# Kernel optimization log

Measured on AMD Instinct MI355X. Metric: run time of the kernel, lower is better.

The kernel has to match this reference:

```python
import jax, jax.numpy as jnp
import numpy as np

B = 16          # number of point clouds
N_COARSE = 1024  # points per cloud at coarse level
N_FINE = 4096    # points per cloud at fine level
C_IN = 256       # coarse feature channels
C_SKIP = 128     # fine skip feature channels
C_HID = 256
EPS = 1e-16


def setup_inputs() -> dict:
    key = jax.random.key(0)
    ks = jax.random.split(key, 8)
    x = jax.random.normal(ks[0], (B * N_COARSE, C_IN), dtype=jnp.float32)
    pos = jax.random.uniform(ks[1], (B * N_COARSE, 3), dtype=jnp.float32)
    x_skip = jax.random.normal(ks[2], (B * N_FINE, C_SKIP), dtype=jnp.float32)
    pos_skip = jax.random.uniform(ks[3], (B * N_FINE, 3), dtype=jnp.float32)
    # uniform batch assignment (sorted), one segment per cloud
    batch = jnp.repeat(jnp.arange(B, dtype=jnp.int32), N_COARSE)
    batch_skip = jnp.repeat(jnp.arange(B, dtype=jnp.int32), N_FINE)
    # MLP params: Linear(384 -> 256) + ReLU, Linear(256 -> 256) + ReLU
    c0 = C_IN + C_SKIP
    W1 = jax.random.normal(ks[4], (c0, C_HID), dtype=jnp.float32) / np.sqrt(c0)
    b1 = jnp.zeros((C_HID,), dtype=jnp.float32)
    W2 = jax.random.normal(ks[5], (C_HID, C_HID), dtype=jnp.float32) / np.sqrt(C_HID)
    b2 = jnp.zeros((C_HID,), dtype=jnp.float32)
    return {"x": x, "pos": pos, "x_skip": x_skip, "pos_skip": pos_skip,
            "W1": W1, "b1": b1, "W2": W2, "b2": b2,
            "batch": batch, "batch_skip": batch_skip, "k": 3}


def _knn_interpolate(x, pos, pos_skip, k):
    # batch is uniform: reshape into [B, n, ...] blocks (same as per-batch kNN)
    xb = x.reshape(B, N_COARSE, -1)          # [B, Nc, C]
    pc = pos.reshape(B, N_COARSE, 3)         # [B, Nc, 3]
    pf = pos_skip.reshape(B, N_FINE, 3)      # [B, Nf, 3]
    # squared pairwise distances within each cloud: [B, Nf, Nc]
    d2 = jnp.sum((pf[:, :, None, :] - pc[:, None, :, :]) ** 2, axis=-1)
    neg_d2, idx = jax.lax.top_k(-d2, k)      # k nearest -> [B, Nf, k]
    w = 1.0 / jnp.maximum(-neg_d2, EPS)      # inverse-squared-distance weights
    gathered = jax.vmap(lambda xc, i: xc[i])(xb, idx)  # [B, Nf, k, C]
    interp = jnp.sum(w[..., None] * gathered, axis=2) / jnp.sum(w, axis=2, keepdims=True)
    return interp.reshape(B * N_FINE, -1)    # [B*Nf, C]


def reference(x, pos, x_skip, pos_skip, W1, b1, W2, b2, batch, batch_skip, k):
    x_up = _knn_interpolate(x, pos, pos_skip, k)
    h = jnp.concatenate([x_up, x_skip], axis=1)          # [B*Nf, C_IN+C_SKIP]
    h = jax.nn.relu(h @ W1 + b1)
    h = jax.nn.relu(h @ W2 + b2)
    return (h, pos_skip, batch_skip)
```

## Files before the change

### kernel.cpp

```cpp
#include <hip/hip_runtime.h>

#define B_ 16
#define NC 1024
#define NF 4096
#define CIN 256
#define CSKIP 128
#define CHID 256
#define MTOT (B_ * NF)
#define EPS_ 1e-16f

typedef _Float16 f16;
typedef __attribute__((ext_vector_type(8))) _Float16 f16x8;
typedef __attribute__((ext_vector_type(4))) _Float16 f16x4;
typedef __attribute__((ext_vector_type(2))) _Float16 f16x2;
typedef __attribute__((ext_vector_type(4))) float f32x4;


__global__ __launch_bounds__(256) void knn_kernel(
    const float* __restrict__ pos, const float* __restrict__ pos_skip,
    int* __restrict__ idx3, float* __restrict__ w3)
{
    __shared__ float4 cpos[NC];
    __shared__ float  cd[64 * 12];
    __shared__ int    ci[64 * 12];

    const int b  = blockIdx.x >> 6;
    const int fb = blockIdx.x & 63;
    const float* cp = pos + (size_t)b * NC * 3;
    for (int i = threadIdx.x; i < NC; i += 256)
        cpos[i] = make_float4(cp[i * 3], cp[i * 3 + 1], cp[i * 3 + 2], 0.0f);
    __syncthreads();

    const int fl = threadIdx.x & 63;
    const int q  = threadIdx.x >> 6;
    const int f  = b * NF + fb * 64 + fl;
    const float px = pos_skip[f * 3 + 0];
    const float py = pos_skip[f * 3 + 1];
    const float pz = pos_skip[f * 3 + 2];

    float d0 = 3.4e38f, d1 = 3.4e38f, d2 = 3.4e38f;
    int   i0 = 0, i1 = 0, i2 = 0;
    const int jbase = q << 8;
#pragma unroll 4
    for (int jj = 0; jj < 256; ++jj) {
        const int j = jbase + jj;
        float4 c = cpos[j];
        float dx = px - c.x, dy = py - c.y, dz = pz - c.z;
        float d = fmaf(dx, dx, fmaf(dy, dy, dz * dz));
        if (d < d2) {
            if (d < d1) {
                d2 = d1; i2 = i1;
                if (d < d0) { d1 = d0; i1 = i0; d0 = d; i0 = j; }
                else        { d1 = d;  i1 = j; }
            } else { d2 = d; i2 = j; }
        }
    }
    const int cb = fl * 12 + q * 3;
    cd[cb + 0] = d0; cd[cb + 1] = d1; cd[cb + 2] = d2;
    ci[cb + 0] = i0; ci[cb + 1] = i1; ci[cb + 2] = i2;
    __syncthreads();

    if (threadIdx.x < 64) {
        float e0 = 3.4e38f, e1 = 3.4e38f, e2 = 3.4e38f;
        int   j0 = 0, j1 = 0, j2 = 0;
#pragma unroll
        for (int s = 0; s < 12; ++s) {
            const float d = cd[fl * 12 + s];
            const int   j = ci[fl * 12 + s];
            if (d < e2) {
                if (d < e1) {
                    e2 = e1; j2 = j1;
                    if (d < e0) { e1 = e0; j1 = j0; e0 = d; j0 = j; }
                    else        { e1 = d;  j1 = j; }
                } else { e2 = d; j2 = j; }
            }
        }
        float w0 = 1.0f / fmaxf(e0, EPS_);
        float w1 = 1.0f / fmaxf(e1, EPS_);
        float w2 = 1.0f / fmaxf(e2, EPS_);
        float inv = 1.0f / (w0 + w1 + w2);
        idx3[f * 3 + 0] = b * NC + j0;
        idx3[f * 3 + 1] = b * NC + j1;
        idx3[f * 3 + 2] = b * NC + j2;
        w3[f * 3 + 0] = w0 * inv;
        w3[f * 3 + 1] = w1 * inv;
        w3[f * 3 + 2] = w2 * inv;
    }
}

__global__ __launch_bounds__(256) void wconv_kernel(
    const float* __restrict__ W1, const float* __restrict__ W2,
    const float* __restrict__ b1,
    f16* __restrict__ W1aT, f16* __restrict__ W1bT, f16* __restrict__ W2T,
    float* __restrict__ b1p)
{
    const int t = blockIdx.x * 256 + threadIdx.x;
    if (t < 256 * 256) {
        const int k = t >> 8, n = t & 255;
        W1aT[n * 256 + k] = (f16)W1[k * 256 + n];
    } else if (t < 256 * 256 + 128 * 256) {
        const int u = t - 256 * 256;
        const int k = u >> 8, n = u & 255;
        W1bT[n * 128 + k] = (f16)W1[(256 + k) * 256 + n];
    } else if (t < 256 * 256 + 128 * 256 + 256 * 256) {
        const int u = t - 256 * 256 - 128 * 256;
        const int n = u >> 8, j = u & 255;
        const int k = (j & ~63) + ((j & 3) << 4) + ((j >> 2) & 15);
        W2T[n * 256 + j] = (f16)W2[k * 256 + n];
    } else if (t < 256 * 256 + 128 * 256 + 256 * 256 + 256) {
        const int j = t - (256 * 256 + 128 * 256 + 256 * 256);
        const int k = (j & ~63) + ((j & 3) << 4) + ((j >> 2) & 15);
        b1p[j] = b1[k];
    }
}

__device__ __forceinline__ void gload16(const void* g, void* l)
{
    __builtin_amdgcn_global_load_lds(
        (const __attribute__((address_space(1))) unsigned int*)g,
        (__attribute__((address_space(3))) unsigned int*)l, 16, 0, 0);
}

template <int K>
__global__ __launch_bounds__(256, 2) void gemm_regA(
    const float* __restrict__ A, const f16* __restrict__ Bt,
    f16* __restrict__ C)
{
    __shared__ f16 As[128 * 64];
    __shared__ f16 Bs[256 * 64];
    const int tid  = threadIdx.x;
    const int lane = tid & 63;
    const int wid  = tid >> 6;
    const int wr   = wid >> 1, wc = wid & 1;
    const int m0   = blockIdx.x * 128;

    const int srow = tid >> 1;
    const int scg  = tid & 1;
    const int srow_l = lane >> 3;
    const int kch    = (lane & 7) ^ ((lane >> 3) & 7);

    f32x4 acc[4][8] = {};

    for (int k0 = 0; k0 < K; k0 += 64) {
#pragma unroll
        for (int r = 0; r < 8; ++r) {
            const int c = (wid << 3) + r;
            const int row = (c << 3) + srow_l;
            gload16(Bt + (size_t)row * K + k0 + kch * 8,
                    (char*)Bs + (c << 10));
        }
        {
            const float* p = A + (size_t)(m0 + srow) * K + k0 + scg * 32;
            float v[32];
#pragma unroll
            for (int j = 0; j < 8; ++j) {
                float4 a = ((const float4*)p)[j];
                v[j * 4 + 0] = a.x; v[j * 4 + 1] = a.y;
                v[j * 4 + 2] = a.z; v[j * 4 + 3] = a.w;
            }
#pragma unroll
            for (int j = 0; j < 4; ++j) {
                f16x8 hh;
#pragma unroll
                for (int t2 = 0; t2 < 8; ++t2) hh[t2] = (f16)v[j * 8 + t2];
                const int sphys = (scg * 4 + j) ^ (srow & 7);
                *(f16x8*)((char*)As + srow * 128 + sphys * 16) = hh;
            }
        }
        __syncthreads();

#pragma unroll
        for (int h = 0; h < 2; ++h) {
            f16x8 aF[4];
#pragma unroll
            for (int m = 0; m < 4; ++m) {
                const int row  = wr * 64 + m * 16 + (lane & 15);
                const int kg   = (h << 2) + (lane >> 4);
                const int slot = kg ^ (row & 7);
                aF[m] = *(const f16x8*)((const char*)As + row * 128 + slot * 16);
            }
#pragma unroll
            for (int n = 0; n < 8; ++n) {
                const int row  = wc * 128 + n * 16 + (lane & 15);
                const int kg   = (h << 2) + (lane >> 4);
                const int slot = kg ^ (row & 7);
                f16x8 bF = *(const f16x8*)((const char*)Bs + row * 128 + slot * 16);
#pragma unroll
                for (int m = 0; m < 4; ++m)
                    acc[m][n] = __builtin_amdgcn_mfma_f32_16x16x32_f16(
                        aF[m], bF, acc[m][n], 0, 0, 0);
            }
        }
        __syncthreads();
    }

    const int qq = lane & 15;
#pragma unroll
    for (int m = 0; m < 4; ++m) {
        const int rb = wr * 64 + m * 16 + ((lane >> 4) << 2);
#pragma unroll
        for (int r = 0; r < 4; ++r) {
            const int rg = m0 + rb + r;
#pragma unroll
            for (int g = 0; g < 2; ++g) {
                f16x4 hv;
#pragma unroll
                for (int n = 0; n < 4; ++n)
                    hv[n] = (f16)acc[m][g * 4 + n][r];
                *(f16x4*)&C[(size_t)rg * 256 + wc * 128 + g * 64 + qq * 4] = hv;
            }
        }
    }
}

__global__ __launch_bounds__(256) void gather_add_relu_kernel(
    const f16* __restrict__ h1pre, const f16* __restrict__ y,
    const int* __restrict__ idx3, const float* __restrict__ w3,
    const float* __restrict__ b1p, f16* __restrict__ h1)
{
    const int w = threadIdx.x >> 6, l = threadIdx.x & 63;
    const int m = blockIdx.x * 4 + w;
    const int i0 = idx3[m * 3 + 0], i1 = idx3[m * 3 + 1], i2 = idx3[m * 3 + 2];
    const float w0 = w3[m * 3 + 0], w1 = w3[m * 3 + 1], w2 = w3[m * 3 + 2];
    const int c = l * 4;

    f16x4 hp = *(const f16x4*)&h1pre[(size_t)m * 256 + c];
    f16x4 y0 = *(const f16x4*)&y[(size_t)i0 * 256 + c];
    f16x4 y1 = *(const f16x4*)&y[(size_t)i1 * 256 + c];
    f16x4 y2 = *(const f16x4*)&y[(size_t)i2 * 256 + c];
    float4 bv = *(const float4*)&b1p[c];

    f16x4 o;
    o.x = (f16)fmaxf((float)hp.x + w0 * (float)y0.x + w1 * (float)y1.x + w2 * (float)y2.x + bv.x, 0.0f);
    o.y = (f16)fmaxf((float)hp.y + w0 * (float)y0.y + w1 * (float)y1.y + w2 * (float)y2.y + bv.y, 0.0f);
    o.z = (f16)fmaxf((float)hp.z + w0 * (float)y0.z + w1 * (float)y1.z + w2 * (float)y2.z + bv.z, 0.0f);
    o.w = (f16)fmaxf((float)hp.w + w0 * (float)y0.w + w1 * (float)y1.w + w2 * (float)y2.w + bv.w, 0.0f);
    *(f16x4*)&h1[(size_t)m * 256 + c] = o;
}

__global__ __launch_bounds__(256, 2) void gemm2_kernel(
    const f16* __restrict__ A, const f16* __restrict__ Bt,
    const float* __restrict__ bias, float* __restrict__ out)
{
    __shared__ f16 As[128 * 64];
    __shared__ f16 Bs[256 * 64];
    const int tid  = threadIdx.x;
    const int lane = tid & 63;
    const int wid  = tid >> 6;
    const int wr   = wid >> 1, wc = wid & 1;
    const int m0   = blockIdx.x * 128;

    const int srow_l = lane >> 3;
    const int kch    = (lane & 7) ^ ((lane >> 3) & 7);

    f32x4 acc[4][8] = {};

    for (int k0 = 0; k0 < 256; k0 += 64) {
#pragma unroll
        for (int r = 0; r < 4; ++r) {
            const int c = (wid << 2) + r;
            const int row = (c << 3) + srow_l;
            gload16(A + (size_t)(m0 + row) * 256 + k0 + kch * 8,
                    (char*)As + (c << 10));
        }
#pragma unroll
        for (int r = 0; r < 8; ++r) {
            const int c = (wid << 3) + r;
            const int row = (c << 3) + srow_l;
            gload16(Bt + (size_t)row * 256 + k0 + kch * 8,
                    (char*)Bs + (c << 10));
        }
        __syncthreads();

#pragma unroll
        for (int h = 0; h < 2; ++h) {
            f16x8 aF[4];
#pragma unroll
            for (int m = 0; m < 4; ++m) {
                const int row  = wr * 64 + m * 16 + (lane & 15);
                const int kg   = (h << 2) + (lane >> 4);
                const int slot = kg ^ (row & 7);
                aF[m] = *(const f16x8*)((const char*)As + row * 128 + slot * 16);
            }
#pragma unroll
            for (int n = 0; n < 8; ++n) {
                const int row  = wc * 128 + n * 16 + (lane & 15);
                const int kg   = (h << 2) + (lane >> 4);
                const int slot = kg ^ (row & 7);
                f16x8 bF = *(const f16x8*)((const char*)Bs + row * 128 + slot * 16);
#pragma unroll
                for (int m = 0; m < 4; ++m)
                    acc[m][n] = __builtin_amdgcn_mfma_f32_16x16x32_f16(
                        aF[m], bF, acc[m][n], 0, 0, 0);
            }
        }
        __syncthreads();
    }

#pragma unroll
    for (int m = 0; m < 4; ++m) {
#pragma unroll
        for (int n = 0; n < 8; ++n) {
            const int col = wc * 128 + n * 16 + (lane & 15);
            const float bv = bias[col];
#pragma unroll
            for (int r = 0; r < 4; ++r) {
                const int row = m0 + wr * 64 + m * 16 + ((lane >> 4) << 2) + r;
                out[(size_t)row * 256 + col] = fmaxf(acc[m][n][r] + bv, 0.0f);
            }
        }
    }
}

__global__ __launch_bounds__(256) void copy_tail_kernel(
    const float* __restrict__ pos_skip, const int* __restrict__ batch_skip,
    float* __restrict__ out)
{
    const int i = blockIdx.x * 256 + threadIdx.x;
    const int npos = MTOT * 3;
    if (i < npos)               out[i] = pos_skip[i];
    else if (i < npos + MTOT)   out[i] = (float)batch_skip[i - npos];
}

extern "C" void kernel_launch(void* const* d_in, const int* in_sizes, int n_in,
                              void* d_out, int out_size, void* d_ws, size_t ws_size,
                              hipStream_t stream)
{
    const float* x        = (const float*)d_in[0];
    const float* pos      = (const float*)d_in[1];
    const float* x_skip   = (const float*)d_in[2];
    const float* pos_skip = (const float*)d_in[3];
    const float* W1       = (const float*)d_in[4];
    const float* b1       = (const float*)d_in[5];
    const float* W2       = (const float*)d_in[6];
    const float* b2       = (const float*)d_in[7];
    const int*   batch_skip = (const int*)d_in[9];
    float* out = (float*)d_out;

    char* ws = (char*)d_ws;
    int*   idx3  = (int*)ws;
    float* w3    = (float*)(ws + (1u << 20));
    f16*   W1aT  = (f16*)(ws + (2u << 20));
    f16*   W1bT  = (f16*)(ws + (2u << 20) + (256u << 10));
    f16*   W2T   = (f16*)(ws + (2u << 20) + (512u << 10));
    float* b1p   = (float*)(ws + (2u << 20) + (768u << 10));
    f16*   y     = (f16*)(ws + (4u << 20));
    f16*   h1pre = (f16*)(ws + (16u << 20));
    f16*   h1    = (f16*)(ws + (48u << 20));

    knn_kernel<<<MTOT / 64, 256, 0, stream>>>(pos, pos_skip, idx3, w3);
    wconv_kernel<<<641, 256, 0, stream>>>(W1, W2, b1, W1aT, W1bT, W2T, b1p);

    gemm_regA<256><<<B_ * NC / 128, 256, 0, stream>>>(x, W1aT, y);
    gemm_regA<128><<<MTOT / 128, 256, 0, stream>>>(x_skip, W1bT, h1pre);
    gather_add_relu_kernel<<<MTOT / 4, 256, 0, stream>>>(h1pre, y, idx3, w3, b1p, h1);

    gemm2_kernel<<<MTOT / 128, 256, 0, stream>>>(h1, W2T, b2, out);

    copy_tail_kernel<<<1024, 256, 0, stream>>>(pos_skip, batch_skip,
                                               out + (size_t)MTOT * CHID);
}
```

Before: 216.1 us.

## Fuse kNN gather epilogue into skip GEMM and merge small kernels

The skip-feature GEMM now applies the weighted kNN gather of y, the bias and the ReLU in its epilogue. This removes the h1pre intermediate write and read and the separate gather kernel. The kNN, weight conversion and tail copy kernels are merged into one launch with block-index dispatch, cutting launch count from seven to four. The trade-offs are scattered y reads inside the GEMM epilogue, which may add register pressure, and the merged kernel reserving kNN shared memory for every block.

```diff
diff --git a/kernel.cpp b/kernel.cpp
--- a/kernel.cpp
+++ b/kernel.cpp
@@ -12,105 +12,110 @@
 typedef _Float16 f16;
 typedef __attribute__((ext_vector_type(8))) _Float16 f16x8;
 typedef __attribute__((ext_vector_type(4))) _Float16 f16x4;
-typedef __attribute__((ext_vector_type(2))) _Float16 f16x2;
 typedef __attribute__((ext_vector_type(4))) float f32x4;
 
 
-__global__ __launch_bounds__(256) void knn_kernel(
+__global__ __launch_bounds__(256) void misc_kernel(
     const float* __restrict__ pos, const float* __restrict__ pos_skip,
-    int* __restrict__ idx3, float* __restrict__ w3)
+    const int* __restrict__ batch_skip,
+    const float* __restrict__ W1, const float* __restrict__ W2,
+    const float* __restrict__ b1,
+    int* __restrict__ idx3, float* __restrict__ w3,
+    f16* __restrict__ W1aT, f16* __restrict__ W1bT, f16* __restrict__ W2T,
+    float* __restrict__ b1p, float* __restrict__ out_tail)
 {
     __shared__ float4 cpos[NC];
     __shared__ float  cd[64 * 12];
     __shared__ int    ci[64 * 12];
 
-    const int b  = blockIdx.x >> 6;
-    const int fb = blockIdx.x & 63;
-    const float* cp = pos + (size_t)b * NC * 3;
-    for (int i = threadIdx.x; i < NC; i += 256)
-        cpos[i] = make_float4(cp[i * 3], cp[i * 3 + 1], cp[i * 3 + 2], 0.0f);
-    __syncthreads();
-
-    const int fl = threadIdx.x & 63;
-    const int q  = threadIdx.x >> 6;
-    const int f  = b * NF + fb * 64 + fl;
-    const float px = pos_skip[f * 3 + 0];
-    const float py = pos_skip[f * 3 + 1];
-    const float pz = pos_skip[f * 3 + 2];
-
-    float d0 = 3.4e38f, d1 = 3.4e38f, d2 = 3.4e38f;
-    int   i0 = 0, i1 = 0, i2 = 0;
-    const int jbase = q << 8;
+    const int bid = blockIdx.x;
+    if (bid < 1024) {
+        const int b  = bid >> 6;
+        const int fb = bid & 63;
+        const float* cp = pos + (size_t)b * NC * 3;
+        for (int i = threadIdx.x; i < NC; i += 256)
+            cpos[i] = make_float4(cp[i * 3], cp[i * 3 + 1], cp[i * 3 + 2], 0.0f);
+        __syncthreads();
+
+        const int fl = threadIdx.x & 63;
+        const int q  = threadIdx.x >> 6;
+        const int f  = b * NF + fb * 64 + fl;
+        const float px = pos_skip[f * 3 + 0];
+        const float py = pos_skip[f * 3 + 1];
+        const float pz = pos_skip[f * 3 + 2];
+
+        float d0 = 3.4e38f, d1 = 3.4e38f, d2 = 3.4e38f;
+        int   i0 = 0, i1 = 0, i2 = 0;
+        const int jbase = q << 8;
 #pragma unroll 4
-    for (int jj = 0; jj < 256; ++jj) {
-        const int j = jbase + jj;
-        float4 c = cpos[j];
-        float dx = px - c.x, dy = py - c.y, dz = pz - c.z;
-        float d = fmaf(dx, dx, fmaf(dy, dy, dz * dz));
-        if (d < d2) {
-            if (d < d1) {
-                d2 = d1; i2 = i1;
-                if (d < d0) { d1 = d0; i1 = i0; d0 = d; i0 = j; }
-                else        { d1 = d;  i1 = j; }
-            } else { d2 = d; i2 = j; }
-        }
-    }
-    const int cb = fl * 12 + q * 3;
-    cd[cb + 0] = d0; cd[cb + 1] = d1; cd[cb + 2] = d2;
-    ci[cb + 0] = i0; ci[cb + 1] = i1; ci[cb + 2] = i2;
-    __syncthreads();
-
-    if (threadIdx.x < 64) {
-        float e0 = 3.4e38f, e1 = 3.4e38f, e2 = 3.4e38f;
-        int   j0 = 0, j1 = 0, j2 = 0;
-#pragma unroll
-        for (int s = 0; s < 12; ++s) {
-            const float d = cd[fl * 12 + s];
-            const int   j = ci[fl * 12 + s];
-            if (d < e2) {
-                if (d < e1) {
-                    e2 = e1; j2 = j1;
-                    if (d < e0) { e1 = e0; j1 = j0; e0 = d; j0 = j; }
-                    else        { e1 = d;  j1 = j; }
-                } else { e2 = d; j2 = j; }
-            }
-        }
-        float w0 = 1.0f / fmaxf(e0, EPS_);
-        float w1 = 1.0f / fmaxf(e1, EPS_);
-        float w2 = 1.0f / fmaxf(e2, EPS_);
-        float inv = 1.0f / (w0 + w1 + w2);
-        idx3[f * 3 + 0] = b * NC + j0;
-        idx3[f * 3 + 1] = b * NC + j1;
-        idx3[f * 3 + 2] = b * NC + j2;
-        w3[f * 3 + 0] = w0 * inv;
-        w3[f * 3 + 1] = w1 * inv;
-        w3[f * 3 + 2] = w2 * inv;
-    }
-}
-
-__global__ __launch_bounds__(256) void wconv_kernel(
-    const float* __restrict__ W1, const float* __restrict__ W2,
-    const float* __restrict__ b1,
-    f16* __restrict__ W1aT, f16* __restrict__ W1bT, f16* __restrict__ W2T,
-    float* __restrict__ b1p)
-{
-    const int t = blockIdx.x * 256 + threadIdx.x;
-    if (t < 256 * 256) {
-        const int k = t >> 8, n = t & 255;
-        W1aT[n * 256 + k] = (f16)W1[k * 256 + n];
-    } else if (t < 256 * 256 + 128 * 256) {
-        const int u = t - 256 * 256;
-        const int k = u >> 8, n = u & 255;
-        W1bT[n * 128 + k] = (f16)W1[(256 + k) * 256 + n];
-    } else if (t < 256 * 256 + 128 * 256 + 256 * 256) {
-        const int u = t - 256 * 256 - 128 * 256;
-        const int n = u >> 8, j = u & 255;
-        const int k = (j & ~63) + ((j & 3) << 4) + ((j >> 2) & 15);
-        W2T[n * 256 + j] = (f16)W2[k * 256 + n];
-    } else if (t < 256 * 256 + 128 * 256 + 256 * 256 + 256) {
-        const int j = t - (256 * 256 + 128 * 256 + 256 * 256);
-        const int k = (j & ~63) + ((j & 3) << 4) + ((j >> 2) & 15);
-        b1p[j] = b1[k];
+        for (int jj = 0; jj < 256; ++jj) {
+            const int j = jbase + jj;
+            float4 c = cpos[j];
+            float dx = px - c.x, dy = py - c.y, dz = pz - c.z;
+            float d = fmaf(dx, dx, fmaf(dy, dy, dz * dz));
+            if (d < d2) {
+                if (d < d1) {
+                    d2 = d1; i2 = i1;
+                    if (d < d0) { d1 = d0; i1 = i0; d0 = d; i0 = j; }
+                    else        { d1 = d;  i1 = j; }
+                } else { d2 = d; i2 = j; }
+            }
+        }
+        const int cb = fl * 12 + q * 3;
+        cd[cb + 0] = d0; cd[cb + 1] = d1; cd[cb + 2] = d2;
+        ci[cb + 0] = i0; ci[cb + 1] = i1; ci[cb + 2] = i2;
+        __syncthreads();
+
+        if (threadIdx.x < 64) {
+            float e0 = 3.4e38f, e1 = 3.4e38f, e2 = 3.4e38f;
+            int   j0 = 0, j1 = 0, j2 = 0;
+#pragma unroll
+            for (int s = 0; s < 12; ++s) {
+                const float d = cd[fl * 12 + s];
+                const int   j = ci[fl * 12 + s];
+                if (d < e2) {
+                    if (d < e1) {
+                        e2 = e1; j2 = j1;
+                        if (d < e0) { e1 = e0; j1 = j0; e0 = d; j0 = j; }
+                        else        { e1 = d;  j1 = j; }
+                    } else { e2 = d; j2 = j; }
+                }
+            }
+            float w0 = 1.0f / fmaxf(e0, EPS_);
+            float w1 = 1.0f / fmaxf(e1, EPS_);
+            float w2 = 1.0f / fmaxf(e2, EPS_);
+            float inv = 1.0f / (w0 + w1 + w2);
+            idx3[f * 3 + 0] = b * NC + j0;
+            idx3[f * 3 + 1] = b * NC + j1;
+            idx3[f * 3 + 2] = b * NC + j2;
+            w3[f * 3 + 0] = w0 * inv;
+            w3[f * 3 + 1] = w1 * inv;
+            w3[f * 3 + 2] = w2 * inv;
+        }
+    } else if (bid < 1665) {
+        const int t = (bid - 1024) * 256 + threadIdx.x;
+        if (t < 256 * 256) {
+            const int k = t >> 8, n = t & 255;
+            W1aT[n * 256 + k] = (f16)W1[k * 256 + n];
+        } else if (t < 256 * 256 + 128 * 256) {
+            const int u = t - 256 * 256;
+            const int k = u >> 8, n = u & 255;
+            W1bT[n * 128 + k] = (f16)W1[(256 + k) * 256 + n];
+        } else if (t < 256 * 256 + 128 * 256 + 256 * 256) {
+            const int u = t - 256 * 256 - 128 * 256;
+            const int n = u >> 8, j = u & 255;
+            const int k = (j & ~63) + ((j & 3) << 4) + ((j >> 2) & 15);
+            W2T[n * 256 + j] = (f16)W2[k * 256 + n];
+        } else if (t < 256 * 256 + 128 * 256 + 256 * 256 + 256) {
+            const int j = t - (256 * 256 + 128 * 256 + 256 * 256);
+            const int k = (j & ~63) + ((j & 3) << 4) + ((j >> 2) & 15);
+            b1p[j] = b1[k];
+        }
+    } else {
+        const int i = (bid - 1665) * 256 + threadIdx.x;
+        const int npos = MTOT * 3;
+        if (i < npos)               out_tail[i] = pos_skip[i];
+        else if (i < npos + MTOT)   out_tail[i] = (float)batch_skip[i - npos];
     }
 }
 
@@ -121,8 +126,7 @@
         (__attribute__((address_space(3))) unsigned int*)l, 16, 0, 0);
 }
 
-template <int K>
-__global__ __launch_bounds__(256, 2) void gemm_regA(
+__global__ __launch_bounds__(256, 2) void gemm_y(
     const float* __restrict__ A, const f16* __restrict__ Bt,
     f16* __restrict__ C)
 {
@@ -141,16 +145,16 @@
 
     f32x4 acc[4][8] = {};
 
-    for (int k0 = 0; k0 < K; k0 += 64) {
+    for (int k0 = 0; k0 < 256; k0 += 64) {
 #pragma unroll
         for (int r = 0; r < 8; ++r) {
             const int c = (wid << 3) + r;
             const int row = (c << 3) + srow_l;
-            gload16(Bt + (size_t)row * K + k0 + kch * 8,
+            gload16(Bt + (size_t)row * 256 + k0 + kch * 8,
                     (char*)Bs + (c << 10));
         }
         {
-            const float* p = A + (size_t)(m0 + srow) * K + k0 + scg * 32;
+            const float* p = A + (size_t)(m0 + srow) * 256 + k0 + scg * 32;
             float v[32];
 #pragma unroll
             for (int j = 0; j < 8; ++j) {
@@ -213,34 +217,11 @@
     }
 }
 
-__global__ __launch_bounds__(256) void gather_add_relu_kernel(
-    const f16* __restrict__ h1pre, const f16* __restrict__ y,
+__global__ __launch_bounds__(256, 2) void gemm1b_fused(
+    const float* __restrict__ A, const f16* __restrict__ Bt,
+    const f16* __restrict__ y,
     const int* __restrict__ idx3, const float* __restrict__ w3,
     const float* __restrict__ b1p, f16* __restrict__ h1)
-{
-    const int w = threadIdx.x >> 6, l = threadIdx.x & 63;
-    const int m = blockIdx.x * 4 + w;
-    const int i0 = idx3[m * 3 + 0], i1 = idx3[m * 3 + 1], i2 = idx3[m * 3 + 2];
-    const float w0 = w3[m * 3 + 0], w1 = w3[m * 3 + 1], w2 = w3[m * 3 + 2];
-    const int c = l * 4;
-
-    f16x4 hp = *(const f16x4*)&h1pre[(size_t)m * 256 + c];
-    f16x4 y0 = *(const f16x4*)&y[(size_t)i0 * 256 + c];
-    f16x4 y1 = *(const f16x4*)&y[(size_t)i1 * 256 + c];
-    f16x4 y2 = *(const f16x4*)&y[(size_t)i2 * 256 + c];
-    float4 bv = *(const float4*)&b1p[c];
-
-    f16x4 o;
-    o.x = (f16)fmaxf((float)hp.x + w0 * (float)y0.x + w1 * (float)y1.x + w2 * (float)y2.x + bv.x, 0.0f);
-    o.y = (f16)fmaxf((float)hp.y + w0 * (float)y0.y + w1 * (float)y1.y + w2 * (float)y2.y + bv.y, 0.0f);
-    o.z = (f16)fmaxf((float)hp.z + w0 * (float)y0.z + w1 * (float)y1.z + w2 * (float)y2.z + bv.z, 0.0f);
-    o.w = (f16)fmaxf((float)hp.w + w0 * (float)y0.w + w1 * (float)y1.w + w2 * (float)y2.w + bv.w, 0.0f);
-    *(f16x4*)&h1[(size_t)m * 256 + c] = o;
-}
-
-__global__ __launch_bounds__(256, 2) void gemm2_kernel(
-    const f16* __restrict__ A, const f16* __restrict__ Bt,
-    const float* __restrict__ bias, float* __restrict__ out)
 {
     __shared__ f16 As[128 * 64];
     __shared__ f16 Bs[256 * 64];
@@ -250,6 +231,110 @@
     const int wr   = wid >> 1, wc = wid & 1;
     const int m0   = blockIdx.x * 128;
 
+    const int srow = tid >> 1;
+    const int scg  = tid & 1;
+    const int srow_l = lane >> 3;
+    const int kch    = (lane & 7) ^ ((lane >> 3) & 7);
+
+    f32x4 acc[4][8] = {};
+
+    for (int k0 = 0; k0 < 128; k0 += 64) {
+#pragma unroll
+        for (int r = 0; r < 8; ++r) {
+            const int c = (wid << 3) + r;
+            const int row = (c << 3) + srow_l;
+            gload16(Bt + (size_t)row * 128 + k0 + kch * 8,
+                    (char*)Bs + (c << 10));
+        }
+        {
+            const float* p = A + (size_t)(m0 + srow) * 128 + k0 + scg * 32;
+            float v[32];
+#pragma unroll
+            for (int j = 0; j < 8; ++j) {
+                float4 a = ((const float4*)p)[j];
+                v[j * 4 + 0] = a.x; v[j * 4 + 1] = a.y;
+                v[j * 4 + 2] = a.z; v[j * 4 + 3] = a.w;
+            }
+#pragma unroll
+            for (int j = 0; j < 4; ++j) {
+                f16x8 hh;
+#pragma unroll
+                for (int t2 = 0; t2 < 8; ++t2) hh[t2] = (f16)v[j * 8 + t2];
+                const int sphys = (scg * 4 + j) ^ (srow & 7);
+                *(f16x8*)((char*)As + srow * 128 + sphys * 16) = hh;
+            }
+        }
+        __syncthreads();
+
+#pragma unroll
+        for (int h = 0; h < 2; ++h) {
+            f16x8 aF[4];
+#pragma unroll
+            for (int m = 0; m < 4; ++m) {
+                const int row  = wr * 64 + m * 16 + (lane & 15);
+                const int kg   = (h << 2) + (lane >> 4);
+                const int slot = kg ^ (row & 7);
+                aF[m] = *(const f16x8*)((const char*)As + row * 128 + slot * 16);
+            }
+#pragma unroll
+            for (int n = 0; n < 8; ++n) {
+                const int row  = wc * 128 + n * 16 + (lane & 15);
+                const int kg   = (h << 2) + (lane >> 4);
+                const int slot = kg ^ (row & 7);
+                f16x8 bF = *(const f16x8*)((const char*)Bs + row * 128 + slot * 16);
+#pragma unroll
+                for (int m = 0; m < 4; ++m)
+                    acc[m][n] = __builtin_amdgcn_mfma_f32_16x16x32_f16(
+                        aF[m], bF, acc[m][n], 0, 0, 0);
+            }
+        }
+        __syncthreads();
+    }
+
+    const int qq = lane & 15;
+    const f32x4 bv0 = *(const f32x4*)&b1p[wc * 128 + qq * 4];
+    const f32x4 bv1 = *(const f32x4*)&b1p[wc * 128 + 64 + qq * 4];
+#pragma unroll
+    for (int m = 0; m < 4; ++m) {
+        const int rb = wr * 64 + m * 16 + ((lane >> 4) << 2);
+#pragma unroll
+        for (int r = 0; r < 4; ++r) {
+            const int rg = m0 + rb + r;
+            const int i0 = idx3[rg * 3 + 0], i1 = idx3[rg * 3 + 1], i2 = idx3[rg * 3 + 2];
+            const float w0 = w3[rg * 3 + 0], w1 = w3[rg * 3 + 1], w2 = w3[rg * 3 + 2];
+#pragma unroll
+            for (int g = 0; g < 2; ++g) {
+                const int jb = wc * 128 + g * 64 + qq * 4;
+                f16x4 y0 = *(const f16x4*)&y[(size_t)i0 * 256 + jb];
+                f16x4 y1 = *(const f16x4*)&y[(size_t)i1 * 256 + jb];
+                f16x4 y2 = *(const f16x4*)&y[(size_t)i2 * 256 + jb];
+                const f32x4 bv = g ? bv1 : bv0;
+                f16x4 hv;
+#pragma unroll
+                for (int n = 0; n < 4; ++n) {
+                    float v = acc[m][g * 4 + n][r]
+                            + w0 * (float)y0[n] + w1 * (float)y1[n] + w2 * (float)y2[n]
+                            + bv[n];
+                    hv[n] = (f16)fmaxf(v, 0.0f);
+                }
+                *(f16x4*)&h1[(size_t)rg * 256 + jb] = hv;
+            }
+        }
+    }
+}
+
+__global__ __launch_bounds__(256, 2) void gemm2_kernel(
+    const f16* __restrict__ A, const f16* __restrict__ Bt,
+    const float* __restrict__ bias, float* __restrict__ out)
+{
+    __shared__ f16 As[128 * 64];
+    __shared__ f16 Bs[256 * 64];
+    const int tid  = threadIdx.x;
+    const int lane = tid & 63;
+    const int wid  = tid >> 6;
+    const int wr   = wid >> 1, wc = wid & 1;
+    const int m0   = blockIdx.x * 128;
+
     const int srow_l = lane >> 3;
     const int kch    = (lane & 7) ^ ((lane >> 3) & 7);
 
@@ -310,16 +395,6 @@
             }
         }
     }
-}
-
-__global__ __launch_bounds__(256) void copy_tail_kernel(
-    const float* __restrict__ pos_skip, const int* __restrict__ batch_skip,
-    float* __restrict__ out)
-{
-    const int i = blockIdx.x * 256 + threadIdx.x;
-    const int npos = MTOT * 3;
-    if (i < npos)               out[i] = pos_skip[i];
-    else if (i < npos + MTOT)   out[i] = (float)batch_skip[i - npos];
 }
 
 extern "C" void kernel_launch(void* const* d_in, const int* in_sizes, int n_in,
@@ -345,18 +420,15 @@
     f16*   W2T   = (f16*)(ws + (2u << 20) + (512u << 10));
     float* b1p   = (float*)(ws + (2u << 20) + (768u << 10));
     f16*   y     = (f16*)(ws + (4u << 20));
-    f16*   h1pre = (f16*)(ws + (16u << 20));
-    f16*   h1    = (f16*)(ws + (48u << 20));
-
-    knn_kernel<<<MTOT / 64, 256, 0, stream>>>(pos, pos_skip, idx3, w3);
-    wconv_kernel<<<641, 256, 0, stream>>>(W1, W2, b1, W1aT, W1bT, W2T, b1p);
-
-    gemm_regA<256><<<B_ * NC / 128, 256, 0, stream>>>(x, W1aT, y);
-    gemm_regA<128><<<MTOT / 128, 256, 0, stream>>>(x_skip, W1bT, h1pre);
-    gather_add_relu_kernel<<<MTOT / 4, 256, 0, stream>>>(h1pre, y, idx3, w3, b1p, h1);
+    f16*   h1    = (f16*)(ws + (16u << 20));
+
+    misc_kernel<<<2689, 256, 0, stream>>>(
+        pos, pos_skip, batch_skip, W1, W2, b1,
+        idx3, w3, W1aT, W1bT, W2T, b1p, out + (size_t)MTOT * CHID);
+
+    gemm_y<<<B_ * NC / 128, 256, 0, stream>>>(x, W1aT, y);
+
+    gemm1b_fused<<<MTOT / 128, 256, 0, stream>>>(x_skip, W1bT, y, idx3, w3, b1p, h1);
 
     gemm2_kernel<<<MTOT / 128, 256, 0, stream>>>(h1, W2T, b2, out);
-
-    copy_tail_kernel<<<1024, 256, 0, stream>>>(pos_skip, batch_skip,
-                                               out + (size_t)MTOT * CHID);
-}
+}
```

After: 199.0 us. 7.9% less time.
